# Kernel optimization log

Hardware: AMD Instinct MI355X
Metric: run time of the kernel (lower is better)

## Reference

```python
import jax, jax.numpy as jnp
import numpy as np

EPS = 1e-7

def segment_softmax(logits, seg, num_segments):
    # Numerically-stable softmax over edges grouped by destination node,
    # applied independently per feature column (logits: [E, D]).
    m = jax.ops.segment_max(logits, seg, num_segments=num_segments)  # [N, D]
    e = jnp.exp(logits - m[seg])                                     # [E, D]
    s = jax.ops.segment_sum(e, seg, num_segments=num_segments)       # [N, D]
    return e / s[seg]

def setup_inputs() -> dict:
    key = jax.random.key(0)
    N, E, D_IN, D_OUT = 50000, 800000, 64, 64
    ks = jax.random.split(key, 4)
    x = jax.random.normal(ks[0], (N, D_IN), dtype=jnp.float32)
    edge_index = jax.random.randint(ks[1], (2, E), 0, N, dtype=jnp.int64)
    # nn.Linear(in_feat, out_feat) params
    W = jax.random.normal(ks[2], (D_OUT, D_IN), dtype=jnp.float32) * (1.0 / np.sqrt(D_IN))
    b = jax.random.normal(ks[3], (D_OUT,), dtype=jnp.float32) * 0.01
    beta = jnp.ones((1,), dtype=jnp.float32)  # aggr='softmax_sg' beta parameter
    return {"x": x, "W": W, "b": b, "beta": beta, "edge_index": edge_index}

def reference(x, W, b, beta, edge_index):
    N = x.shape[0]
    dst = edge_index[0]  # scatter / softmax segment ids
    src = edge_index[1]  # gather ids
    # gather + ReLU + eps
    edge_msg = jax.nn.relu(x[src]) + EPS                    # [E, D]
    # softmax_sg aggregation: softmax of beta*msg over incoming edges of each dst
    a = segment_softmax(beta * edge_msg, dst, N)            # [E, D]
    h = jax.ops.segment_sum(edge_msg * a, dst, num_segments=N)  # [N, D]
    # final Linear
    return h @ W.T + b
```

## Files before the change

kernel.cpp:

```cpp
#include <hip/hip_runtime.h>
#include <hip/hip_fp16.h>

#define EPS 1e-7f
#define EPB 4096
#define CSTRIDE 16
#define HS 68

__device__ __forceinline__ void pack_body(const float4* __restrict__ x4,
                                          short4* __restrict__ xh, int i, int hi) {
    if (i < hi) {
        float4 v = x4[i];
        short4 o;
        o.x = __half_as_short(__float2half_rn(fmaxf(v.x, 0.f) + EPS));
        o.y = __half_as_short(__float2half_rn(fmaxf(v.y, 0.f) + EPS));
        o.z = __half_as_short(__float2half_rn(fmaxf(v.z, 0.f) + EPS));
        o.w = __half_as_short(__float2half_rn(fmaxf(v.w, 0.f) + EPS));
        xh[i] = o;
    }
}

__global__ __launch_bounds__(256) void part_kernel(const float4* __restrict__ x4,
                                                   short4* __restrict__ xh, int nq,
                                                   int eblocks,
                                                   const int* __restrict__ ei, int E,
                                                   int CAPB,
                                                   int* __restrict__ cursor,
                                                   unsigned int* __restrict__ partArr) {
    int bb = blockIdx.x;
    int tid = threadIdx.x;
    if (bb == 0 && tid < 16) {
        short fbff = (short)0xFBFF;
        xh[nq + tid] = make_short4(fbff, fbff, fbff, fbff);
    }
    if (bb >= eblocks) {
        pack_body(x4, xh, (bb - eblocks) * 256 + tid, nq);
        return;
    }
    __shared__ int hist[256];
    __shared__ int off[256];
    hist[tid] = 0;
    __syncthreads();

    int base = bb * EPB;
    int dd[16], ss[16], bk[16], rk[16];
    #pragma unroll
    for (int k = 0; k < 16; ++k) {
        int e = base + k * 256 + tid;
        bk[k] = -1;
        if (e < E) {
            dd[k] = ei[e];
            ss[k] = ei[E + e];
            bk[k] = dd[k] >> 8;
            rk[k] = atomicAdd(&hist[bk[k]], 1);
        }
    }
    __syncthreads();
    int hv = hist[tid];
    if (hv > 0) off[tid] = atomicAdd(&cursor[tid * CSTRIDE], hv);
    __syncthreads();
    #pragma unroll
    for (int k = 0; k < 16; ++k) {
        if (bk[k] >= 0) {
            int idx = off[bk[k]] + rk[k];
            if (idx < CAPB)
                partArr[(size_t)bk[k] * CAPB + idx] =
                    ((unsigned int)dd[k] << 16) | (unsigned int)(ss[k] & 0xFFFF);
        }
    }
}

#if __has_builtin(__builtin_amdgcn_exp2f)
#define EXPB(m) __builtin_amdgcn_exp2f(bl2 * (m))
#else
#define EXPB(m) __expf(beta * (m))
#endif
__global__ __launch_bounds__(512) void main_kernel(const unsigned int* __restrict__ partArr,
                                                   const int* __restrict__ cursor,
                                                   int CAPB,
                                                   const __half* __restrict__ xh,
                                                   const float* __restrict__ beta_p,
                                                   const float* __restrict__ W,
                                                   const float* __restrict__ bias,
                                                   float* __restrict__ out, int N,
                                                   int cq, int cr) {
    __shared__ float hl[32 * HS];
    __shared__ float Wt[64 * HS];
    __shared__ unsigned short sl[32 * 64];
    __shared__ int hist[32];
    int tid  = threadIdx.x;
    int bid  = blockIdx.x;
    int x = bid & 7, jj = bid >> 3;
    int m = ((x < cr) ? x * (cq + 1) : cr * (cq + 1) + (x - cr) * cq) + jj;
    int n0 = m << 5;
    int bkt = m >> 3;

    if (tid < 32) hist[tid] = 0;

    #pragma unroll
    for (int kk = 0; kk < 2; ++kk) {
        int i4 = kk * 512 + tid;
        int rj = i4 >> 4;
        int d0 = (i4 & 15) * 4;
        float4 wv = *(const float4*)(W + (size_t)i4 * 4);
        Wt[(d0 + 0) * HS + rj] = wv.x;
        Wt[(d0 + 1) * HS + rj] = wv.y;
        Wt[(d0 + 2) * HS + rj] = wv.z;
        Wt[(d0 + 3) * HS + rj] = wv.w;
    }
    __syncthreads();

    int cnt = cursor[bkt * CSTRIDE];
    if (cnt > CAPB) cnt = CAPB;
    const unsigned int* pa = partArr + (size_t)bkt * CAPB;
    for (int i = tid; i < cnt; i += 512) {
        unsigned int u = pa[i];
        int rel = (int)(u >> 16) - n0;
        if ((unsigned)rel < 32u) {
            int rr = atomicAdd(&hist[rel], 1);
            if (rr < 64) sl[(rel << 6) + rr] = (unsigned short)(u & 0xFFFF);
        }
    }
    __syncthreads();

    int lane = tid & 63;
    int w    = tid >> 6;
    float beta = beta_p[0];
    float bl2  = beta * 1.44269504088896f;
    int la0 = w << 2;
    int dq0 = hist[la0 + 0], dq1 = hist[la0 + 1];
    int dq2 = hist[la0 + 2], dq3 = hist[la0 + 3];
    if (dq0 > 64) dq0 = 64;
    if (dq1 > 64) dq1 = 64;
    if (dq2 > 64) dq2 = 64;
    if (dq3 > 64) dq3 = 64;
    int id0 = (lane < dq0) ? (int)sl[((la0 + 0) << 6) + lane] : N;
    int id1 = (lane < dq1) ? (int)sl[((la0 + 1) << 6) + lane] : N;
    int id2 = (lane < dq2) ? (int)sl[((la0 + 2) << 6) + lane] : N;
    int id3 = (lane < dq3) ? (int)sl[((la0 + 3) << 6) + lane] : N;

    #pragma unroll
    for (int pp = 0; pp < 2; ++pp) {
        const int idA = pp ? id2 : id0;
        const int idB = pp ? id3 : id1;
        const int dgA = pp ? dq2 : dq0;
        const int dgB = pp ? dq3 : dq1;
        int la = la0 + (pp << 1);
        int dgm = (dgA > dgB) ? dgA : dgB;

        float sA = 0.f, tA = 0.f, sB = 0.f, tB = 0.f;
        #define ACCV(wv, sX, tX) { float mm = __half2float(wv);                 \
            float e = EXPB(mm);                \
            sX += e; tX = fmaf(mm, e, tX); }
        for (int i = 0; i < dgm; i += 8) {
            const __half* a0 = xh + (__builtin_amdgcn_readlane(idA, i + 0) << 6);
            const __half* a1 = xh + (__builtin_amdgcn_readlane(idA, i + 1) << 6);
            const __half* a2 = xh + (__builtin_amdgcn_readlane(idA, i + 2) << 6);
            const __half* a3 = xh + (__builtin_amdgcn_readlane(idA, i + 3) << 6);
            const __half* a4 = xh + (__builtin_amdgcn_readlane(idA, i + 4) << 6);
            const __half* a5 = xh + (__builtin_amdgcn_readlane(idA, i + 5) << 6);
            const __half* a6 = xh + (__builtin_amdgcn_readlane(idA, i + 6) << 6);
            const __half* a7 = xh + (__builtin_amdgcn_readlane(idA, i + 7) << 6);
            const __half* b0 = xh + (__builtin_amdgcn_readlane(idB, i + 0) << 6);
            const __half* b1 = xh + (__builtin_amdgcn_readlane(idB, i + 1) << 6);
            const __half* b2 = xh + (__builtin_amdgcn_readlane(idB, i + 2) << 6);
            const __half* b3 = xh + (__builtin_amdgcn_readlane(idB, i + 3) << 6);
            const __half* b4 = xh + (__builtin_amdgcn_readlane(idB, i + 4) << 6);
            const __half* b5 = xh + (__builtin_amdgcn_readlane(idB, i + 5) << 6);
            const __half* b6 = xh + (__builtin_amdgcn_readlane(idB, i + 6) << 6);
            const __half* b7 = xh + (__builtin_amdgcn_readlane(idB, i + 7) << 6);
            __half wa0 = a0[lane], wa1 = a1[lane], wa2 = a2[lane], wa3 = a3[lane];
            __half wa4 = a4[lane], wa5 = a5[lane], wa6 = a6[lane], wa7 = a7[lane];
            __half wb0 = b0[lane], wb1 = b1[lane], wb2 = b2[lane], wb3 = b3[lane];
            __half wb4 = b4[lane], wb5 = b5[lane], wb6 = b6[lane], wb7 = b7[lane];
            ACCV(wa0, sA, tA) ACCV(wa1, sA, tA) ACCV(wa2, sA, tA) ACCV(wa3, sA, tA)
            ACCV(wa4, sA, tA) ACCV(wa5, sA, tA) ACCV(wa6, sA, tA) ACCV(wa7, sA, tA)
            ACCV(wb0, sB, tB) ACCV(wb1, sB, tB) ACCV(wb2, sB, tB) ACCV(wb3, sB, tB)
            ACCV(wb4, sB, tB) ACCV(wb5, sB, tB) ACCV(wb6, sB, tB) ACCV(wb7, sB, tB)
        }
        #undef ACCV
        hl[la * HS + lane]       = (dgA > 0) ? (tA / sA) : 0.0f;
        hl[(la + 1) * HS + lane] = (dgB > 0) ? (tB / sB) : 0.0f;
    }
    __syncthreads();

    int c4 = tid & 15;
    int r  = tid >> 4;
    float4 bv = *(const float4*)(bias + c4 * 4);
    float a0 = bv.x, a1 = bv.y, a2 = bv.z, a3 = bv.w;
    const float* hrow = hl + r * HS;
    const float* wcol = Wt + c4 * 4;
    #pragma unroll 4
    for (int d4 = 0; d4 < 16; ++d4) {
        float4 hv  = *(const float4*)(hrow + d4 * 4);
        float4 w0v = *(const float4*)(wcol + (d4 * 4 + 0) * HS);
        float4 w1v = *(const float4*)(wcol + (d4 * 4 + 1) * HS);
        float4 w2v = *(const float4*)(wcol + (d4 * 4 + 2) * HS);
        float4 w3v = *(const float4*)(wcol + (d4 * 4 + 3) * HS);
        a0 = fmaf(hv.x, w0v.x, a0); a1 = fmaf(hv.x, w0v.y, a1);
        a2 = fmaf(hv.x, w0v.z, a2); a3 = fmaf(hv.x, w0v.w, a3);
        a0 = fmaf(hv.y, w1v.x, a0); a1 = fmaf(hv.y, w1v.y, a1);
        a2 = fmaf(hv.y, w1v.z, a2); a3 = fmaf(hv.y, w1v.w, a3);
        a0 = fmaf(hv.z, w2v.x, a0); a1 = fmaf(hv.z, w2v.y, a1);
        a2 = fmaf(hv.z, w2v.z, a2); a3 = fmaf(hv.z, w2v.w, a3);
        a0 = fmaf(hv.w, w3v.x, a0); a1 = fmaf(hv.w, w3v.y, a1);
        a2 = fmaf(hv.w, w3v.z, a2); a3 = fmaf(hv.w, w3v.w, a3);
    }
    int row = n0 + r;
    if (row < N)
        *(float4*)(out + (size_t)row * 64 + c4 * 4) = make_float4(a0, a1, a2, a3);
}

extern "C" void kernel_launch(void* const* d_in, const int* in_sizes, int n_in,
                              void* d_out, int out_size, void* d_ws, size_t ws_size,
                              hipStream_t stream) {
    const float* x      = (const float*)d_in[0];
    const float* W      = (const float*)d_in[1];
    const float* b      = (const float*)d_in[2];
    const float* beta_p = (const float*)d_in[3];
    const int*   ei     = (const int*)d_in[4];

    int NT = in_sizes[0];
    int N  = NT / 64;
    int E  = in_sizes[4] / 2;
    int nq = NT / 4;

    int NBK = (N + 255) >> 8;
    int eblocks = (E + EPB - 1) / EPB;
    int pblocks = (nq + 255) / 256;
    int nblk = (N + 31) / 32;
    int cq = nblk / 8, cr = nblk % 8;

    size_t curB   = (size_t)NBK * CSTRIDE * 4;
    size_t xhB    = (size_t)NT * 2 + 128;
    size_t fixedB = curB + xhB;
    int CAPB = (int)(((size_t)2 * E / NBK + 255) & ~(size_t)255);
    if (ws_size < fixedB + (size_t)NBK * CAPB * 4) {
        size_t avail = (ws_size > fixedB) ? (ws_size - fixedB) : 0;
        int fitc = (int)(avail / ((size_t)NBK * 4));
        CAPB = (fitc / 64) * 64;
        if (CAPB <= 0) return;
    }

    char* p = (char*)d_ws;
    int* cursor           = (int*)p;              p += curB;
    unsigned int* partArr = (unsigned int*)p;     p += (size_t)NBK * CAPB * 4;
    __half* xh            = (__half*)p;

    hipMemsetAsync(cursor, 0, curB, stream);

    part_kernel<<<eblocks + pblocks, 256, 0, stream>>>(
        (const float4*)x, (short4*)xh, nq, eblocks, ei, E, CAPB, cursor, partArr);

    main_kernel<<<nblk, 512, 0, stream>>>(partArr, cursor, CAPB, xh, beta_p,
                                          W, b, (float*)d_out, N, cq, cr);
}
```

Baseline: 121.8 us.

## Partition edges into 32-node buckets so each main block reads only its own

The edge partition now uses buckets of 32 destination nodes (one per main-kernel block) instead of 256, so each main block scans only its own bucket instead of filtering 8x more edges. The per-block histogram in the partition kernel grows to up to 2048 shared entries, the global cursor atomics become more numerous and more contended, and the XCD-aware block remapping is removed. Per-bucket capacity CAPB shrinks proportionally, and the 2x slack over the mean count is tighter relative to variance at the smaller bucket size, so overflow could silently drop edges.

```diff
diff --git a/kernel.cpp b/kernel.cpp
--- a/kernel.cpp
+++ b/kernel.cpp
@@ -5,6 +5,8 @@
 #define EPB 4096
 #define CSTRIDE 16
 #define HS 68
+#define BSH 5
+#define MAXBK 2048
 
 __device__ __forceinline__ void pack_body(const float4* __restrict__ x4,
                                           short4* __restrict__ xh, int i, int hi) {
@@ -23,7 +25,7 @@
                                                    short4* __restrict__ xh, int nq,
                                                    int eblocks,
                                                    const int* __restrict__ ei, int E,
-                                                   int CAPB,
+                                                   int NBK, int CAPB,
                                                    int* __restrict__ cursor,
                                                    unsigned int* __restrict__ partArr) {
     int bb = blockIdx.x;
@@ -36,9 +38,9 @@
         pack_body(x4, xh, (bb - eblocks) * 256 + tid, nq);
         return;
     }
-    __shared__ int hist[256];
-    __shared__ int off[256];
-    hist[tid] = 0;
+    __shared__ int hist[MAXBK];
+    __shared__ int off[MAXBK];
+    for (int j = tid; j < NBK; j += 256) hist[j] = 0;
     __syncthreads();
 
     int base = bb * EPB;
@@ -50,13 +52,15 @@
         if (e < E) {
             dd[k] = ei[e];
             ss[k] = ei[E + e];
-            bk[k] = dd[k] >> 8;
+            bk[k] = dd[k] >> BSH;
             rk[k] = atomicAdd(&hist[bk[k]], 1);
         }
     }
     __syncthreads();
-    int hv = hist[tid];
-    if (hv > 0) off[tid] = atomicAdd(&cursor[tid * CSTRIDE], hv);
+    for (int s = tid; s < NBK; s += 256) {
+        int hv = hist[s];
+        if (hv > 0) off[s] = atomicAdd(&cursor[s * CSTRIDE], hv);
+    }
     __syncthreads();
     #pragma unroll
     for (int k = 0; k < 16; ++k) {
@@ -81,18 +85,14 @@
                                                    const float* __restrict__ beta_p,
                                                    const float* __restrict__ W,
                                                    const float* __restrict__ bias,
-                                                   float* __restrict__ out, int N,
-                                                   int cq, int cr) {
+                                                   float* __restrict__ out, int N) {
     __shared__ float hl[32 * HS];
     __shared__ float Wt[64 * HS];
     __shared__ unsigned short sl[32 * 64];
     __shared__ int hist[32];
     int tid  = threadIdx.x;
     int bid  = blockIdx.x;
-    int x = bid & 7, jj = bid >> 3;
-    int m = ((x < cr) ? x * (cq + 1) : cr * (cq + 1) + (x - cr) * cq) + jj;
-    int n0 = m << 5;
-    int bkt = m >> 3;
+    int n0   = bid << 5;
 
     if (tid < 32) hist[tid] = 0;
 
@@ -109,9 +109,9 @@
     }
     __syncthreads();
 
-    int cnt = cursor[bkt * CSTRIDE];
+    int cnt = cursor[bid * CSTRIDE];
     if (cnt > CAPB) cnt = CAPB;
-    const unsigned int* pa = partArr + (size_t)bkt * CAPB;
+    const unsigned int* pa = partArr + (size_t)bid * CAPB;
     for (int i = tid; i < cnt; i += 512) {
         unsigned int u = pa[i];
         int rel = (int)(u >> 16) - n0;
@@ -224,11 +224,10 @@
     int E  = in_sizes[4] / 2;
     int nq = NT / 4;
 
-    int NBK = (N + 255) >> 8;
+    int NBK = (N + 31) >> BSH;
+    if (NBK > MAXBK) return;
     int eblocks = (E + EPB - 1) / EPB;
     int pblocks = (nq + 255) / 256;
-    int nblk = (N + 31) / 32;
-    int cq = nblk / 8, cr = nblk % 8;
 
     size_t curB   = (size_t)NBK * CSTRIDE * 4;
     size_t xhB    = (size_t)NT * 2 + 128;
@@ -249,8 +248,9 @@
     hipMemsetAsync(cursor, 0, curB, stream);
 
     part_kernel<<<eblocks + pblocks, 256, 0, stream>>>(
-        (const float4*)x, (short4*)xh, nq, eblocks, ei, E, CAPB, cursor, partArr);
-
-    main_kernel<<<nblk, 512, 0, stream>>>(partArr, cursor, CAPB, xh, beta_p,
-                                          W, b, (float*)d_out, N, cq, cr);
-}
+        (const float4*)x, (short4*)xh, nq, eblocks, ei, E, NBK, CAPB,
+        cursor, partArr);
+
+    main_kernel<<<NBK, 512, 0, stream>>>(partArr, cursor, CAPB, xh, beta_p,
+                                         W, b, (float*)d_out, N);
+}
```

New measurement: 130.4 us. 7.1% more time.
